# Performance work log

Hardware: AMD Instinct MI355X
Metric: run time of the kernel (lower is better)

Reference implementation:

```python
import jax, jax.numpy as jnp
import numpy as np

LN_EPS = 1e-5
LOG_EPS = 1e-8

def _layernorm(x, w, b):
    mu = jnp.mean(x, axis=-1, keepdims=True)
    var = jnp.mean((x - mu) ** 2, axis=-1, keepdims=True)
    return (x - mu) * jax.lax.rsqrt(var + LN_EPS) * w + b


def setup_inputs() -> dict:
    key = jax.random.key(0)
    ks = jax.random.split(key, 8)
    B, T, D = 4, 4096, 1024
    x = jax.random.normal(ks[0], (B, T, D), dtype=jnp.float32)
    ln_w = jnp.ones((D,), jnp.float32)
    ln_b = jnp.zeros((D,), jnp.float32)
    # torch Linear stores weight as (out, in)
    Wf = jax.random.normal(ks[1], (D, D), jnp.float32) / np.sqrt(D)
    bf = jax.random.normal(ks[2], (D,), jnp.float32) * 0.02
    # module inits reach to zeros; use small random values for a non-trivial baseline
    Wr = jax.random.normal(ks[3], (D, D), jnp.float32) * 0.02
    br = jax.random.normal(ks[4], (D,), jnp.float32) * 0.02
    alpha_bias = jnp.array([3.0], jnp.float32) + jax.random.normal(ks[5], (1,), jnp.float32) * 0.1
    beta_scale = jnp.array([0.02], jnp.float32)
    return {"x": x, "ln_w": ln_w, "ln_b": ln_b, "Wf": Wf, "bf": bf,
            "Wr": Wr, "br": br, "alpha_bias": alpha_bias, "beta_scale": beta_scale}


def reference(x, ln_w, ln_b, Wf, bf, Wr, br, alpha_bias, beta_scale):
    residual = x
    x_norm = _layernorm(x, ln_w, ln_b)                       # [B,T,D]
    alpha = jax.nn.sigmoid(jnp.einsum('btd,ed->bte', x_norm, Wf) + bf + alpha_bias)
    beta_x = beta_scale * (1.0 - alpha) * x_norm
    log_alpha = jnp.log(alpha + LOG_EPS)
    log_alpha_cumsum = jnp.cumsum(log_alpha, axis=1)          # [B,T,D]
    m = jnp.max(log_alpha_cumsum, axis=1, keepdims=True)      # [B,1,D]
    scale = jnp.exp(log_alpha_cumsum - m)
    x_star = beta_x * scale
    s_star = jnp.cumsum(x_star, axis=1)
    output = s_star / (scale + LOG_EPS)
    x_gate = jnp.tanh(jnp.einsum('btd,ed->bte', output, Wr) + br)
    return x_gate * 0.05 + residual
```

## Files before the change

### kernel.cpp

```cpp
#include <hip/hip_runtime.h>

#define D_DIM 1024
#define B_DIM 4
#define T_DIM 4096
#define M_DIM (B_DIM * T_DIM)
#define CHUNK 32
#define NCHUNK (T_DIM / CHUNK)
#define SEG (NCHUNK / 4)

typedef unsigned short u16;
typedef __attribute__((ext_vector_type(8))) unsigned short us8;
typedef __attribute__((ext_vector_type(8))) __bf16 bf16x8;
typedef __attribute__((ext_vector_type(4))) float f32x4;

__device__ __forceinline__ float bf2f(u16 u) {
    union { unsigned int i; float f; } v;
    v.i = ((unsigned int)u) << 16;
    return v.f;
}
__device__ __forceinline__ u16 f2bf(float f) {
    union { float f; unsigned int i; } v;
    v.f = f;
    unsigned int u = v.i;
    unsigned int r = (u + 0x7fffu + ((u >> 16) & 1u)) >> 16;
    return (u16)r;
}
__device__ __forceinline__ float fast_tanh(float v) {
    float e = __expf(2.f * v);
    return 1.f - 2.f / (e + 1.f);
}

#define GLOAD16(g, l)                                                   \
    __builtin_amdgcn_global_load_lds(                                   \
        (const __attribute__((address_space(1))) void*)(g),             \
        (__attribute__((address_space(3))) void*)(l), 16, 0, 0)

__global__ __launch_bounds__(256) void conv2_kernel(const float* __restrict__ a,
                                                    const float* __restrict__ b,
                                                    u16* __restrict__ da,
                                                    u16* __restrict__ db) {
    int i = blockIdx.x * 256 + threadIdx.x;
    const float* s = (i < 262144) ? a : b;
    u16* dp = (i < 262144) ? da : db;
    int j = i & 262143;
    float4 v = ((const float4*)s)[j];
    ushort4 o;
    o.x = f2bf(v.x); o.y = f2bf(v.y); o.z = f2bf(v.z); o.w = f2bf(v.w);
    ((ushort4*)dp)[j] = o;
}

__global__ __launch_bounds__(256) void ln_kernel(const float* __restrict__ x,
                                                 const float* __restrict__ w,
                                                 const float* __restrict__ b,
                                                 u16* __restrict__ xn) {
    __shared__ float red[8];
    int row = blockIdx.x;
    int tid = threadIdx.x;
    float4 v = ((const float4*)(x + (size_t)row * D_DIM))[tid];
    float s  = v.x + v.y + v.z + v.w;
    float s2 = v.x * v.x + v.y * v.y + v.z * v.z + v.w * v.w;
    #pragma unroll
    for (int o = 32; o > 0; o >>= 1) {
        s  += __shfl_xor(s, o, 64);
        s2 += __shfl_xor(s2, o, 64);
    }
    int wave = tid >> 6, lane = tid & 63;
    if (lane == 0) { red[wave] = s; red[wave + 4] = s2; }
    __syncthreads();
    if (tid == 0) {
        float ts  = red[0] + red[1] + red[2] + red[3];
        float ts2 = red[4] + red[5] + red[6] + red[7];
        float mu  = ts * (1.0f / D_DIM);
        float var = ts2 * (1.0f / D_DIM) - mu * mu;
        red[0] = mu;
        red[1] = rsqrtf(var + 1e-5f);
    }
    __syncthreads();
    float mu = red[0], rs = red[1];
    float4 wv = ((const float4*)w)[tid];
    float4 bv = ((const float4*)b)[tid];
    ushort4 o;
    o.x = f2bf((v.x - mu) * rs * wv.x + bv.x);
    o.y = f2bf((v.y - mu) * rs * wv.y + bv.y);
    o.z = f2bf((v.z - mu) * rs * wv.z + bv.z);
    o.w = f2bf((v.w - mu) * rs * wv.w + bv.w);
    ((ushort4*)(xn + (size_t)row * D_DIM))[tid] = o;
}

template <int EPI>
__global__ __launch_bounds__(256) void gemm_kernel(const u16* __restrict__ A,
                                                   const u16* __restrict__ Bm,
                                                   const float* __restrict__ bias,
                                                   const float* __restrict__ resid,
                                                   const float* __restrict__ sc0,
                                                   u16* __restrict__ out_bf,
                                                   float* __restrict__ out_f) {
    __shared__ __align__(16) u16 lds_a[128 * 32];
    __shared__ __align__(16) u16 lds_b[128 * 32];
    int tid  = threadIdx.x;
    int wave = tid >> 6, lane = tid & 63;
    int tile_n = blockIdx.x * 128;
    int tile_m = blockIdx.y * 128;
    int wr = wave >> 1, wc = wave & 1;

    f32x4 acc[4][4] = {};

    int srow = wave * 32 + (lane >> 2);
    int scol = (lane & 3) * 8;
    const u16* ga0 = A  + (size_t)(tile_m + srow) * D_DIM + scol;
    const u16* ga1 = ga0 + 16 * D_DIM;
    const u16* gb0 = Bm + (size_t)(tile_n + srow) * D_DIM + scol;
    const u16* gb1 = gb0 + 16 * D_DIM;
    u16* la0 = &lds_a[(wave * 32) * 32];
    u16* la1 = &lds_a[(wave * 32 + 16) * 32];
    u16* lb0 = &lds_b[(wave * 32) * 32];
    u16* lb1 = &lds_b[(wave * 32 + 16) * 32];

    for (int k0 = 0; k0 < D_DIM; k0 += 32) {
        GLOAD16(ga0 + k0, la0);
        GLOAD16(ga1 + k0, la1);
        GLOAD16(gb0 + k0, lb0);
        GLOAD16(gb1 + k0, lb1);
        __syncthreads();

        bf16x8 af[4], bfr[4];
        #pragma unroll
        for (int mi = 0; mi < 4; mi++) {
            int m = wr * 64 + mi * 16 + (lane & 15);
            af[mi] = *(const bf16x8*)&lds_a[m * 32 + (lane >> 4) * 8];
        }
        #pragma unroll
        for (int ni = 0; ni < 4; ni++) {
            int n = wc * 64 + ni * 16 + (lane & 15);
            bfr[ni] = *(const bf16x8*)&lds_b[n * 32 + (lane >> 4) * 8];
        }
        #pragma unroll
        for (int mi = 0; mi < 4; mi++)
            #pragma unroll
            for (int ni = 0; ni < 4; ni++)
                acc[mi][ni] = __builtin_amdgcn_mfma_f32_16x16x32_bf16(
                    af[mi], bfr[ni], acc[mi][ni], 0, 0, 0);
        __syncthreads();
    }

    if constexpr (EPI == 0) {
        float abv = sc0[0];
        #pragma unroll
        for (int mi = 0; mi < 4; mi++) {
            #pragma unroll
            for (int r = 0; r < 4; r++) {
                int row = tile_m + wr * 64 + mi * 16 + (lane >> 4) * 4 + r;
                #pragma unroll
                for (int ni = 0; ni < 4; ni++) {
                    int col = tile_n + wc * 64 + ni * 16 + (lane & 15);
                    size_t idx = (size_t)row * D_DIM + col;
                    float z = acc[mi][ni][r] + bias[col] + abv;
                    float alpha = 1.f / (1.f + __expf(-z));
                    out_bf[idx] = f2bf(__logf(alpha + 1e-8f));
                }
            }
        }
    } else {
        #pragma unroll
        for (int mi = 0; mi < 4; mi++) {
            #pragma unroll
            for (int r = 0; r < 4; r++) {
                int row = tile_m + wr * 64 + mi * 16 + (lane >> 4) * 4 + r;
                #pragma unroll
                for (int ni = 0; ni < 4; ni++) {
                    int col = tile_n + wc * 64 + ni * 16 + (lane & 15);
                    size_t idx = (size_t)row * D_DIM + col;
                    float g = fast_tanh(acc[mi][ni][r] + bias[col]);
                    out_f[idx] = 0.05f * g + resid[idx];
                }
            }
        }
    }
}

__global__ __launch_bounds__(256) void scan_chunk(const u16* __restrict__ la,
                                                  const u16* __restrict__ xn,
                                                  const float* __restrict__ bs,
                                                  float* __restrict__ S,
                                                  float* __restrict__ Ml,
                                                  float* __restrict__ Tb) {
    int bc = blockIdx.x;
    int b = bc >> 7, c = bc & (NCHUNK - 1);
    int d = blockIdx.y * 256 + threadIdx.x;
    float bsv = bs[0];
    size_t base = ((size_t)(b * T_DIM + c * CHUNK)) * D_DIM + d;
    float p[CHUNK];
    float run = 0.f, mx = -3.4e38f;
    #pragma unroll
    for (int t = 0; t < CHUNK; t++) {
        run += bf2f(la[base + (size_t)t * D_DIM]);
        p[t] = run;
        mx = fmaxf(mx, run);
    }
    float tb = 0.f;
    #pragma unroll
    for (int t = 0; t < CHUNK; t++) {
        size_t idx = base + (size_t)t * D_DIM;
        float lav = bf2f(la[idx]);
        float bx = bsv * (-expm1f(lav)) * bf2f(xn[idx]);
        tb += bx * __expf(p[t] - mx);
    }
    size_t ci = ((size_t)(b * NCHUNK + c)) * D_DIM + d;
    S[ci] = run; Ml[ci] = mx; Tb[ci] = tb;
}

__global__ __launch_bounds__(256) void scan_combine(const float* __restrict__ S,
                                                    const float* __restrict__ Ml,
                                                    const float* __restrict__ Tb,
                                                    float* __restrict__ Of,
                                                    float* __restrict__ SSp) {
    __shared__ float lsS[4][64], lsM[4][64], lsW[4][64];
    int b = blockIdx.x >> 4;
    int dg = blockIdx.x & 15;
    int wave = threadIdx.x >> 6, lane = threadIdx.x & 63;
    int d = dg * 64 + lane;
    size_t base = ((size_t)b * NCHUNK) * D_DIM + d;
    int c0 = wave * SEG;

    float O = 0.f, m = -3.4e38f;
    for (int j = 0; j < SEG; j++) {
        size_t ci = base + (size_t)(c0 + j) * D_DIM;
        m = fmaxf(m, O + Ml[ci]);
        O += S[ci];
    }
    lsS[wave][lane] = O; lsM[wave][lane] = m;
    __syncthreads();

    float myOsup = 0.f, gm = -3.4e38f;
    {
        float o = 0.f;
        #pragma unroll
        for (int w2 = 0; w2 < 4; w2++) {
            if (w2 == wave) myOsup = o;
            gm = fmaxf(gm, o + lsM[w2][lane]);
            o += lsS[w2][lane];
        }
    }

    float wv[SEG];
    float wacc = 0.f, Oc = myOsup;
    for (int j = 0; j < SEG; j++) {
        size_t ci = base + (size_t)(c0 + j) * D_DIM;
        Of[ci] = Oc - gm;
        float wcj = __expf(Oc + Ml[ci] - gm) * Tb[ci];
        wv[j] = wacc;
        wacc += wcj;
        Oc += S[ci];
    }
    lsW[wave][lane] = wacc;
    __syncthreads();

    float ssup = 0.f;
    #pragma unroll
    for (int w2 = 0; w2 < 4; w2++)
        if (w2 < wave) ssup += lsW[w2][lane];

    for (int j = 0; j < SEG; j++) {
        size_t ci = base + (size_t)(c0 + j) * D_DIM;
        SSp[ci] = ssup + wv[j];
    }
}

__global__ __launch_bounds__(256) void scan_final(const u16* __restrict__ la,
                                                  const u16* __restrict__ xn,
                                                  const float* __restrict__ bs,
                                                  const float* __restrict__ Of,
                                                  const float* __restrict__ SSp,
                                                  u16* __restrict__ osc) {
    int bc = blockIdx.x;
    int b = bc >> 7, c = bc & (NCHUNK - 1);
    int d = blockIdx.y * 256 + threadIdx.x;
    float bsv = bs[0];
    size_t base = ((size_t)(b * T_DIM + c * CHUNK)) * D_DIM + d;
    size_t ci = ((size_t)(b * NCHUNK + c)) * D_DIM + d;
    float ofs = Of[ci], ss = SSp[ci], p = 0.f;
    #pragma unroll
    for (int t = 0; t < CHUNK; t++) {
        size_t idx = base + (size_t)t * D_DIM;
        float lav = bf2f(la[idx]);
        p += lav;
        float scv = __expf(ofs + p);
        float bx = bsv * (-expm1f(lav)) * bf2f(xn[idx]);
        ss += bx * scv;
        osc[idx] = f2bf(ss / (scv + 1e-8f));
    }
}

extern "C" void kernel_launch(void* const* d_in, const int* in_sizes, int n_in,
                              void* d_out, int out_size, void* d_ws, size_t ws_size,
                              hipStream_t stream) {
    const float* x   = (const float*)d_in[0];
    const float* lnw = (const float*)d_in[1];
    const float* lnb = (const float*)d_in[2];
    const float* Wf  = (const float*)d_in[3];
    const float* bf_ = (const float*)d_in[4];
    const float* Wr  = (const float*)d_in[5];
    const float* br  = (const float*)d_in[6];
    const float* ab  = (const float*)d_in[7];
    const float* bs  = (const float*)d_in[8];
    float* out = (float*)d_out;

    char* w = (char*)d_ws;
    u16* xn  = (u16*)w;
    u16* la  = (u16*)(w + (size_t)33554432);
    u16* Wfc = (u16*)(w + (size_t)67108864);
    u16* Wrc = (u16*)(w + (size_t)69206016);
    float* S   = (float*)(w + (size_t)71303168);
    float* Ml  = S  + 524288;
    float* Tb  = Ml + 524288;
    float* Of  = Tb + 524288;
    float* SSp = Of + 524288;
    u16* osc = xn;

    conv2_kernel<<<dim3(2048), dim3(256), 0, stream>>>(Wf, Wr, Wfc, Wrc);
    ln_kernel<<<dim3(M_DIM), dim3(256), 0, stream>>>(x, lnw, lnb, xn);
    gemm_kernel<0><<<dim3(D_DIM / 128, M_DIM / 128), dim3(256), 0, stream>>>(
        xn, Wfc, bf_, nullptr, ab, la, nullptr);
    scan_chunk<<<dim3(B_DIM * NCHUNK, 4), dim3(256), 0, stream>>>(la, xn, bs, S, Ml, Tb);
    scan_combine<<<dim3(B_DIM * 16), dim3(256), 0, stream>>>(S, Ml, Tb, Of, SSp);
    scan_final<<<dim3(B_DIM * NCHUNK, 4), dim3(256), 0, stream>>>(la, xn, bs, Of, SSp, osc);
    gemm_kernel<1><<<dim3(D_DIM / 128, M_DIM / 128), dim3(256), 0, stream>>>(
        osc, Wrc, br, x, nullptr, nullptr, out);
}
```

Baseline: 307.6 us.

## Fuse weight conversion into layernorm, vectorize scans, widen scan combine to 16 waves

Merges the weight-to-bf16 conversion kernel into the layernorm kernel so there is one fewer launch. The chunk and final scan kernels now have each thread handle four adjacent columns with ushort4 loads and stores, which cuts the grid by four and widens memory accesses. The chunk scan recomputes the prefix instead of keeping a 32-entry register array. scan_combine now uses 1024 threads (16 waves) to shorten each wave's serial segment, and expm1f is replaced with 1-__expf, which loses some accuracy for small values.

```diff
diff --git a/kernel.cpp b/kernel.cpp
--- a/kernel.cpp
+++ b/kernel.cpp
@@ -6,7 +6,8 @@
 #define M_DIM (B_DIM * T_DIM)
 #define CHUNK 32
 #define NCHUNK (T_DIM / CHUNK)
-#define SEG (NCHUNK / 4)
+#define NWAVE_C 16
+#define SEG (NCHUNK / NWAVE_C)
 
 typedef unsigned short u16;
 typedef __attribute__((ext_vector_type(8))) unsigned short us8;
@@ -35,27 +36,28 @@
         (const __attribute__((address_space(1))) void*)(g),             \
         (__attribute__((address_space(3))) void*)(l), 16, 0, 0)
 
-__global__ __launch_bounds__(256) void conv2_kernel(const float* __restrict__ a,
-                                                    const float* __restrict__ b,
-                                                    u16* __restrict__ da,
-                                                    u16* __restrict__ db) {
-    int i = blockIdx.x * 256 + threadIdx.x;
-    const float* s = (i < 262144) ? a : b;
-    u16* dp = (i < 262144) ? da : db;
-    int j = i & 262143;
-    float4 v = ((const float4*)s)[j];
-    ushort4 o;
-    o.x = f2bf(v.x); o.y = f2bf(v.y); o.z = f2bf(v.z); o.w = f2bf(v.w);
-    ((ushort4*)dp)[j] = o;
-}
-
-__global__ __launch_bounds__(256) void ln_kernel(const float* __restrict__ x,
-                                                 const float* __restrict__ w,
-                                                 const float* __restrict__ b,
-                                                 u16* __restrict__ xn) {
+__global__ __launch_bounds__(256) void ln_conv_kernel(const float* __restrict__ x,
+                                                      const float* __restrict__ w,
+                                                      const float* __restrict__ b,
+                                                      u16* __restrict__ xn,
+                                                      const float* __restrict__ Wf,
+                                                      const float* __restrict__ Wr,
+                                                      u16* __restrict__ da,
+                                                      u16* __restrict__ db) {
     __shared__ float red[8];
-    int row = blockIdx.x;
     int tid = threadIdx.x;
+    if (blockIdx.x < 2048) {
+        int i = blockIdx.x * 256 + tid;
+        const float* s = (i < 262144) ? Wf : Wr;
+        u16* dp = (i < 262144) ? da : db;
+        int j = i & 262143;
+        float4 v = ((const float4*)s)[j];
+        ushort4 o;
+        o.x = f2bf(v.x); o.y = f2bf(v.y); o.z = f2bf(v.z); o.w = f2bf(v.w);
+        ((ushort4*)dp)[j] = o;
+        return;
+    }
+    int row = blockIdx.x - 2048;
     float4 v = ((const float4*)(x + (size_t)row * D_DIM))[tid];
     float s  = v.x + v.y + v.z + v.w;
     float s2 = v.x * v.x + v.y * v.y + v.z * v.z + v.w * v.w;
@@ -186,35 +188,49 @@
                                                   float* __restrict__ Tb) {
     int bc = blockIdx.x;
     int b = bc >> 7, c = bc & (NCHUNK - 1);
-    int d = blockIdx.y * 256 + threadIdx.x;
+    int col0 = threadIdx.x * 4;
     float bsv = bs[0];
-    size_t base = ((size_t)(b * T_DIM + c * CHUNK)) * D_DIM + d;
-    float p[CHUNK];
-    float run = 0.f, mx = -3.4e38f;
-    #pragma unroll
+    size_t base = ((size_t)(b * T_DIM + c * CHUNK)) * D_DIM + col0;
+    float run[4], mx[4];
+    #pragma unroll
+    for (int j = 0; j < 4; j++) { run[j] = 0.f; mx[j] = -3.4e38f; }
+    #pragma unroll 4
     for (int t = 0; t < CHUNK; t++) {
-        run += bf2f(la[base + (size_t)t * D_DIM]);
-        p[t] = run;
-        mx = fmaxf(mx, run);
-    }
-    float tb = 0.f;
-    #pragma unroll
+        ushort4 v = *(const ushort4*)(la + base + (size_t)t * D_DIM);
+        run[0] += bf2f(v.x); mx[0] = fmaxf(mx[0], run[0]);
+        run[1] += bf2f(v.y); mx[1] = fmaxf(mx[1], run[1]);
+        run[2] += bf2f(v.z); mx[2] = fmaxf(mx[2], run[2]);
+        run[3] += bf2f(v.w); mx[3] = fmaxf(mx[3], run[3]);
+    }
+    float tb[4], p[4];
+    #pragma unroll
+    for (int j = 0; j < 4; j++) { tb[j] = 0.f; p[j] = 0.f; }
+    #pragma unroll 4
     for (int t = 0; t < CHUNK; t++) {
         size_t idx = base + (size_t)t * D_DIM;
-        float lav = bf2f(la[idx]);
-        float bx = bsv * (-expm1f(lav)) * bf2f(xn[idx]);
-        tb += bx * __expf(p[t] - mx);
-    }
-    size_t ci = ((size_t)(b * NCHUNK + c)) * D_DIM + d;
-    S[ci] = run; Ml[ci] = mx; Tb[ci] = tb;
-}
-
-__global__ __launch_bounds__(256) void scan_combine(const float* __restrict__ S,
-                                                    const float* __restrict__ Ml,
-                                                    const float* __restrict__ Tb,
-                                                    float* __restrict__ Of,
-                                                    float* __restrict__ SSp) {
-    __shared__ float lsS[4][64], lsM[4][64], lsW[4][64];
+        ushort4 lv = *(const ushort4*)(la + idx);
+        ushort4 xv = *(const ushort4*)(xn + idx);
+        u16 lvs[4] = {lv.x, lv.y, lv.z, lv.w};
+        u16 xvs[4] = {xv.x, xv.y, xv.z, xv.w};
+        #pragma unroll
+        for (int j = 0; j < 4; j++) {
+            float lav = bf2f(lvs[j]);
+            p[j] += lav;
+            float bx = bsv * (1.f - __expf(lav)) * bf2f(xvs[j]);
+            tb[j] += bx * __expf(p[j] - mx[j]);
+        }
+    }
+    size_t ci = ((size_t)(b * NCHUNK + c)) * D_DIM + col0;
+    #pragma unroll
+    for (int j = 0; j < 4; j++) { S[ci + j] = run[j]; Ml[ci + j] = mx[j]; Tb[ci + j] = tb[j]; }
+}
+
+__global__ __launch_bounds__(1024) void scan_combine(const float* __restrict__ S,
+                                                     const float* __restrict__ Ml,
+                                                     const float* __restrict__ Tb,
+                                                     float* __restrict__ Of,
+                                                     float* __restrict__ SSp) {
+    __shared__ float lsS[NWAVE_C][64], lsM[NWAVE_C][64], lsW[NWAVE_C][64];
     int b = blockIdx.x >> 4;
     int dg = blockIdx.x & 15;
     int wave = threadIdx.x >> 6, lane = threadIdx.x & 63;
@@ -223,6 +239,7 @@
     int c0 = wave * SEG;
 
     float O = 0.f, m = -3.4e38f;
+    #pragma unroll
     for (int j = 0; j < SEG; j++) {
         size_t ci = base + (size_t)(c0 + j) * D_DIM;
         m = fmaxf(m, O + Ml[ci]);
@@ -235,7 +252,7 @@
     {
         float o = 0.f;
         #pragma unroll
-        for (int w2 = 0; w2 < 4; w2++) {
+        for (int w2 = 0; w2 < NWAVE_C; w2++) {
             if (w2 == wave) myOsup = o;
             gm = fmaxf(gm, o + lsM[w2][lane]);
             o += lsS[w2][lane];
@@ -244,6 +261,7 @@
 
     float wv[SEG];
     float wacc = 0.f, Oc = myOsup;
+    #pragma unroll
     for (int j = 0; j < SEG; j++) {
         size_t ci = base + (size_t)(c0 + j) * D_DIM;
         Of[ci] = Oc - gm;
@@ -257,9 +275,10 @@
 
     float ssup = 0.f;
     #pragma unroll
-    for (int w2 = 0; w2 < 4; w2++)
+    for (int w2 = 0; w2 < NWAVE_C; w2++)
         if (w2 < wave) ssup += lsW[w2][lane];
 
+    #pragma unroll
     for (int j = 0; j < SEG; j++) {
         size_t ci = base + (size_t)(c0 + j) * D_DIM;
         SSp[ci] = ssup + wv[j];
@@ -274,20 +293,33 @@
                                                   u16* __restrict__ osc) {
     int bc = blockIdx.x;
     int b = bc >> 7, c = bc & (NCHUNK - 1);
-    int d = blockIdx.y * 256 + threadIdx.x;
+    int col0 = threadIdx.x * 4;
     float bsv = bs[0];
-    size_t base = ((size_t)(b * T_DIM + c * CHUNK)) * D_DIM + d;
-    size_t ci = ((size_t)(b * NCHUNK + c)) * D_DIM + d;
-    float ofs = Of[ci], ss = SSp[ci], p = 0.f;
-    #pragma unroll
+    size_t base = ((size_t)(b * T_DIM + c * CHUNK)) * D_DIM + col0;
+    size_t ci = ((size_t)(b * NCHUNK + c)) * D_DIM + col0;
+    float ofs[4], ss[4], p[4];
+    #pragma unroll
+    for (int j = 0; j < 4; j++) { ofs[j] = Of[ci + j]; ss[j] = SSp[ci + j]; p[j] = 0.f; }
+    #pragma unroll 4
     for (int t = 0; t < CHUNK; t++) {
         size_t idx = base + (size_t)t * D_DIM;
-        float lav = bf2f(la[idx]);
-        p += lav;
-        float scv = __expf(ofs + p);
-        float bx = bsv * (-expm1f(lav)) * bf2f(xn[idx]);
-        ss += bx * scv;
-        osc[idx] = f2bf(ss / (scv + 1e-8f));
+        ushort4 lv = *(const ushort4*)(la + idx);
+        ushort4 xv = *(const ushort4*)(xn + idx);
+        u16 lvs[4] = {lv.x, lv.y, lv.z, lv.w};
+        u16 xvs[4] = {xv.x, xv.y, xv.z, xv.w};
+        ushort4 o;
+        u16 os[4];
+        #pragma unroll
+        for (int j = 0; j < 4; j++) {
+            float lav = bf2f(lvs[j]);
+            p[j] += lav;
+            float scv = __expf(ofs[j] + p[j]);
+            float bx = bsv * (1.f - __expf(lav)) * bf2f(xvs[j]);
+            ss[j] += bx * scv;
+            os[j] = f2bf(ss[j] / (scv + 1e-8f));
+        }
+        o.x = os[0]; o.y = os[1]; o.z = os[2]; o.w = os[3];
+        *(ushort4*)(osc + idx) = o;
     }
 }
 
@@ -317,13 +349,13 @@
     float* SSp = Of + 524288;
     u16* osc = xn;
 
-    conv2_kernel<<<dim3(2048), dim3(256), 0, stream>>>(Wf, Wr, Wfc, Wrc);
-    ln_kernel<<<dim3(M_DIM), dim3(256), 0, stream>>>(x, lnw, lnb, xn);
+    ln_conv_kernel<<<dim3(2048 + M_DIM), dim3(256), 0, stream>>>(
+        x, lnw, lnb, xn, Wf, Wr, Wfc, Wrc);
     gemm_kernel<0><<<dim3(D_DIM / 128, M_DIM / 128), dim3(256), 0, stream>>>(
         xn, Wfc, bf_, nullptr, ab, la, nullptr);
-    scan_chunk<<<dim3(B_DIM * NCHUNK, 4), dim3(256), 0, stream>>>(la, xn, bs, S, Ml, Tb);
-    scan_combine<<<dim3(B_DIM * 16), dim3(256), 0, stream>>>(S, Ml, Tb, Of, SSp);
-    scan_final<<<dim3(B_DIM * NCHUNK, 4), dim3(256), 0, stream>>>(la, xn, bs, Of, SSp, osc);
+    scan_chunk<<<dim3(B_DIM * NCHUNK), dim3(256), 0, stream>>>(la, xn, bs, S, Ml, Tb);
+    scan_combine<<<dim3(B_DIM * 16), dim3(1024), 0, stream>>>(S, Ml, Tb, Of, SSp);
+    scan_final<<<dim3(B_DIM * NCHUNK), dim3(256), 0, stream>>>(la, xn, bs, Of, SSp, osc);
     gemm_kernel<1><<<dim3(D_DIM / 128, M_DIM / 128), dim3(256), 0, stream>>>(
         osc, Wrc, br, x, nullptr, nullptr, out);
 }
```

Result: no change. 308.1 us (+0.2%).
